# Optimization experiments

Measured on AMD Instinct MI355X. Metric: run time of the kernel, lower is better.

## Reference

```python
import jax, jax.numpy as jnp
import numpy as np

N, E = 50000, 200000
SIZES = [16, 32, 16]
EDIM = 8
EPS = 1e-5


def setup_inputs() -> dict:
    key = jax.random.key(0)
    ks = jax.random.split(key, 16)
    inp = {
        "x": jax.random.normal(ks[0], (N, SIZES[0]), jnp.float32),
        "edge_attr": jax.random.normal(ks[1], (E, EDIM), jnp.float32),
        "edge_index": jax.random.randint(ks[2], (2, E), 0, N, dtype=jnp.int32),
    }
    ki = 3
    for l in range(2):
        fin, fout = SIZES[l], SIZES[l + 1]
        m = fin * fout
        # xavier-ish init matching torch.nn.init.xavier_uniform_ scales
        inp[f"W1_{l}"] = jax.random.normal(ks[ki], (EDIM, m), jnp.float32) / np.float32(np.sqrt(EDIM)); ki += 1
        inp[f"b1_{l}"] = jnp.zeros((m,), jnp.float32)
        inp[f"W2_{l}"] = jax.random.normal(ks[ki], (m, m), jnp.float32) * np.float32(0.01 / np.sqrt(m)); ki += 1
        inp[f"b2_{l}"] = jnp.zeros((m,), jnp.float32)
        inp[f"root_{l}"] = jax.random.normal(ks[ki], (fin, fout), jnp.float32) / np.float32(np.sqrt(fin)); ki += 1
        inp[f"bias_{l}"] = jnp.zeros((fout,), jnp.float32)
        inp[f"gamma_{l}"] = jnp.ones((fout,), jnp.float32)
        inp[f"beta_{l}"] = jnp.zeros((fout,), jnp.float32)
    return inp


def _lrelu(v):
    return jnp.where(v >= 0, v, 0.01 * v)


def _nnconv(x, src, dst, edge_attr, W1, b1, W2, b2, root, bias, fin, fout):
    # edge MLP -> per-edge weight matrix [E, fin, fout]
    h = _lrelu(edge_attr @ W1 + b1) @ W2 + b2
    h = h.reshape(-1, fin, fout)
    # gather source node features, tiny per-edge matmul
    msg = jnp.einsum('ei,eio->eo', x[src], h)  # [E, fout]
    # scatter-mean aggregate at destination nodes
    agg = jax.ops.segment_sum(msg, dst, num_segments=N)
    deg = jax.ops.segment_sum(jnp.ones((msg.shape[0],), msg.dtype), dst, num_segments=N)
    agg = agg / jnp.maximum(deg, 1.0)[:, None]
    return agg + x @ root + bias


def _bn(v, gamma, beta):
    # BatchNorm1d (training mode: batch stats, biased variance)
    mu = v.mean(0)
    var = v.var(0)
    return (v - mu) * jax.lax.rsqrt(var + EPS) * gamma + beta


def reference(x, edge_attr,
              W1_0, b1_0, W2_0, b2_0, root_0, bias_0, gamma_0, beta_0,
              W1_1, b1_1, W2_1, b2_1, root_1, bias_1, gamma_1, beta_1,
              edge_index):
    src, dst = edge_index[0], edge_index[1]
    h = _nnconv(x, src, dst, edge_attr, W1_0, b1_0, W2_0, b2_0, root_0, bias_0, SIZES[0], SIZES[1])
    h = _lrelu(_bn(h, gamma_0, beta_0))
    h = _nnconv(h, src, dst, edge_attr, W1_1, b1_1, W2_1, b2_1, root_1, bias_1, SIZES[1], SIZES[2])
    return _bn(h, gamma_1, beta_1)
```

## Files before the change

kernel.cpp:

```cpp
#include <hip/hip_runtime.h>
#include <hip/hip_bf16.h>

typedef __attribute__((ext_vector_type(4))) float f32x4;
typedef __attribute__((ext_vector_type(8))) short s16x8;
typedef __attribute__((ext_vector_type(4))) int int4v;

#define DEVI __device__ __forceinline__

constexpr int NN = 50000;
constexpr int NE = 200000;
constexpr float BN_EPS = 1e-5f;

DEVI float lrelu_f(float v) { return v >= 0.f ? v : 0.01f * v; }

__global__ void k_transpose_w2(const float* __restrict__ W2, __hip_bfloat16* __restrict__ W2T) {
  __shared__ float tile[32][33];
  int bx = blockIdx.x % 16, by = blockIdx.x / 16;
  int t = threadIdx.x;
  int r = t / 32, c = t % 32;
  for (int rr = r; rr < 32; rr += 8)
    tile[rr][c] = W2[(size_t)(by * 32 + rr) * 512 + bx * 32 + c];
  __syncthreads();
  for (int rr = r; rr < 32; rr += 8)
    W2T[(size_t)(bx * 32 + rr) * 512 + by * 32 + c] = __float2bfloat16(tile[c][rr]);
}

__global__ void k_transpose_w1(const float* __restrict__ W1, __hip_bfloat16* __restrict__ W1T) {
  int tid = blockIdx.x * 256 + threadIdx.x;
  if (tid < 8 * 512) {
    int k = tid / 512, n = tid % 512;
    W1T[n * 8 + k] = __float2bfloat16(W1[tid]);
  }
}

__global__ void k_count(const int* __restrict__ dst, int* __restrict__ cnt) {
  int e = blockIdx.x * 256 + threadIdx.x;
  if (e < NE) atomicAdd(&cnt[dst[e]], 1);
}

constexpr int SCAN_ELEMS = 1024;
__global__ void k_scan1(const int* __restrict__ cnt, int* __restrict__ base, int* __restrict__ aux, int n) {
  __shared__ int sw[256];
  int b = blockIdx.x, t = threadIdx.x;
  int i0 = b * SCAN_ELEMS + t * 4;
  int v[4]; int s = 0;
  #pragma unroll
  for (int j = 0; j < 4; j++) { int idx = i0 + j; v[j] = (idx < n) ? cnt[idx] : 0; s += v[j]; }
  sw[t] = s; __syncthreads();
  for (int d = 1; d < 256; d <<= 1) {
    int val = (t >= d) ? sw[t - d] : 0;
    __syncthreads();
    sw[t] += val;
    __syncthreads();
  }
  int run = (t > 0) ? sw[t - 1] : 0;
  #pragma unroll
  for (int j = 0; j < 4; j++) { int idx = i0 + j; if (idx < n) base[idx] = run; run += v[j]; }
  if (t == 255) aux[b] = sw[255];
}

__global__ void k_scan2(int* aux, int nb) {
  if (threadIdx.x == 0 && blockIdx.x == 0) {
    int run = 0;
    for (int i = 0; i < nb; i++) { int v = aux[i]; aux[i] = run; run += v; }
  }
}

__global__ void k_scan3(int* __restrict__ base, int* __restrict__ cursor, const int* __restrict__ aux, int n) {
  int i = blockIdx.x * 256 + threadIdx.x;
  if (i < n) { int v = base[i] + aux[i / SCAN_ELEMS]; base[i] = v; cursor[i] = v; }
}

__global__ void k_place(const int* __restrict__ dst, int* __restrict__ cursor, int* __restrict__ perm) {
  int e = blockIdx.x * 256 + threadIdx.x;
  if (e < NE) { int p = atomicAdd(&cursor[dst[e]], 1); perm[p] = e; }
}

template <int FIN, int FOUT>
__global__ __launch_bounds__(512, 2)
void k_edge(const float* __restrict__ x, const float* __restrict__ ea,
            const int* __restrict__ srcI,
            const __hip_bfloat16* __restrict__ W1T, const float* __restrict__ b1,
            const __hip_bfloat16* __restrict__ W2T, const float* __restrict__ b2,
            __hip_bfloat16* __restrict__ msgb)
{
  static_assert(FOUT == 32 || FOUT == 16, "");
  constexpr int TM = 256;
  constexpr int CG = 32;
  constexpr int NCGI = 512 / CG;
  constexpr int NKC = 8;
  constexpr int NOT = FOUT / 16;
  constexpr int XPAD = 4;

  __shared__ __align__(16) char bbuf[2][CG * 512 * 2];
  __shared__ __align__(16) char gbuf[8][32 * 64 * 2];
  __shared__ __align__(16) __hip_bfloat16 eab[TM][8];
  __shared__ __align__(16) float xlf[TM][FIN + XPAD];

  const int tid = threadIdx.x;
  const int lane = tid & 63, w = tid >> 6;
  const int l15 = lane & 15, l4 = lane >> 4;
  const int e0 = blockIdx.x * TM;
  const int rem = min(TM, NE - e0);
  const int wrow0 = w * 32;

  if (tid < TM) {
    int er = e0 + min(tid, rem - 1);
    float4 v0 = *(const float4*)(ea + (size_t)er * 8);
    float4 v1 = *(const float4*)(ea + (size_t)er * 8 + 4);
    __hip_bfloat16* p = &eab[tid][0];
    p[0] = __float2bfloat16(v0.x); p[1] = __float2bfloat16(v0.y);
    p[2] = __float2bfloat16(v0.z); p[3] = __float2bfloat16(v0.w);
    p[4] = __float2bfloat16(v1.x); p[5] = __float2bfloat16(v1.y);
    p[6] = __float2bfloat16(v1.z); p[7] = __float2bfloat16(v1.w);
  }
  {
    constexpr int PRV = FIN / 4;
    for (int v = tid; v < TM * PRV; v += 512) {
      int row = v / PRV, q = v % PRV;
      int er = e0 + min(row, rem - 1);
      int s = srcI[er];
      *(float4*)(&xlf[row][q * 4]) = *(const float4*)(x + (size_t)s * FIN + q * 4);
    }
  }
  __syncthreads();

  s16x8 afe[2];
  #pragma unroll
  for (int rt = 0; rt < 2; rt++) {
    s16x8 tv = *(const s16x8*)(&eab[wrow0 + rt * 16 + l15][0]);
    afe[rt] = (lane < 16) ? tv : (s16x8)0;
  }
  char* gme = gbuf[w];
  s16x8 af[NKC][2][2];
  #pragma unroll
  for (int kc = 0; kc < NKC; kc++) {
    #pragma unroll
    for (int ct = 0; ct < 4; ct++) {
      int c = kc * 64 + ct * 16 + l15;
      s16x8 bw = *(const s16x8*)(W1T + c * 8);
      bw = (lane < 16) ? bw : (s16x8)0;
      float b1v = b1[c];
      #pragma unroll
      for (int rt = 0; rt < 2; rt++) {
        f32x4 d = __builtin_amdgcn_mfma_f32_16x16x32_bf16(afe[rt], bw, (f32x4)(0.f), 0, 0, 0);
        #pragma unroll
        for (int r = 0; r < 4; r++) {
          int rloc = rt * 16 + l4 * 4 + r;
          float gv = d[r] + b1v;
          gv = gv >= 0.f ? gv : 0.01f * gv;
          int byt = (rloc * 128 + (ct * 16 + l15) * 2) ^ ((rloc & 7) << 4);
          *(__hip_bfloat16*)(gme + byt) = __float2bfloat16(gv);
        }
      }
    }
    #pragma unroll
    for (int rt = 0; rt < 2; rt++)
      #pragma unroll
      for (int ks = 0; ks < 2; ks++) {
        int rloc = rt * 16 + l15;
        int byt = (rloc * 128 + (ks * 32 + l4 * 8) * 2) ^ ((rloc & 7) << 4);
        af[kc][rt][ks] = *(const s16x8*)(gme + byt);
      }
  }

  auto stage = [&](int cgi) {
    char* bb = bbuf[cgi & 1];
    int n = tid >> 4;
    int s0 = tid & 15;
    const char* gp = (const char*)(W2T + (size_t)(cgi * CG + n) * 512);
    #pragma unroll
    for (int j = 0; j < 4; j++) {
      int s = s0 + j * 16;
      *(int4v*)(&bb[n * 1024 + ((s ^ (n & 7)) << 4)]) = *(const int4v*)(gp + s * 16);
    }
  };

  f32x4 msg[2][NOT];
  #pragma unroll
  for (int rt = 0; rt < 2; rt++)
    #pragma unroll
    for (int ot = 0; ot < NOT; ot++) msg[rt][ot] = (f32x4)(0.f);

  stage(0);
  __syncthreads();

  for (int cgi = 0; cgi < NCGI; ++cgi) {
    if (cgi + 1 < NCGI) stage(cgi + 1);
    const char* bb = bbuf[cgi & 1];

    f32x4 acc[2][2];
    acc[0][0] = (f32x4)(0.f); acc[0][1] = (f32x4)(0.f);
    acc[1][0] = (f32x4)(0.f); acc[1][1] = (f32x4)(0.f);

    #pragma unroll
    for (int kc = 0; kc < NKC; kc++) {
      #pragma unroll
      for (int ct = 0; ct < 2; ct++) {
        int c = ct * 16 + l15;
        #pragma unroll
        for (int ks = 0; ks < 2; ks++) {
          int k = kc * 64 + ks * 32 + l4 * 8;
          s16x8 bw = *(const s16x8*)(&bb[(c * 1024 + k * 2) ^ ((c & 7) << 4)]);
          #pragma unroll
          for (int rt = 0; rt < 2; rt++)
            acc[rt][ct] = __builtin_amdgcn_mfma_f32_16x16x32_bf16(af[kc][rt][ks], bw, acc[rt][ct], 0, 0, 0);
        }
      }
    }

    #pragma unroll
    for (int ct = 0; ct < 2; ct++) {
      float b2v = b2[cgi * CG + ct * 16 + l15];
      const int iv = (FOUT == 32) ? cgi : (cgi * 2 + ct);
      const int ot = (FOUT == 32) ? ct : 0;
      #pragma unroll
      for (int rt = 0; rt < 2; rt++)
        #pragma unroll
        for (int r = 0; r < 4; r++) {
          int row = wrow0 + rt * 16 + l4 * 4 + r;
          msg[rt][ot][r] += xlf[row][iv] * (acc[rt][ct][r] + b2v);
        }
    }
    __syncthreads();
  }

  #pragma unroll
  for (int rt = 0; rt < 2; rt++)
    #pragma unroll
    for (int r = 0; r < 4; r++) {
      int row = wrow0 + rt * 16 + l4 * 4 + r;
      if (row < rem) {
        #pragma unroll
        for (int ot = 0; ot < NOT; ot++)
          msgb[(size_t)(e0 + row) * FOUT + ot * 16 + l15] = __float2bfloat16(msg[rt][ot][r]);
      }
    }
}

template <int FIN, int FOUT>
__global__ void k_node_agg(const __hip_bfloat16* __restrict__ msgb, const int* __restrict__ perm,
                           const int* __restrict__ base,
                           const float* __restrict__ x,
                           const float* __restrict__ root,
                           const float* __restrict__ bias,
                           float* __restrict__ h)
{
  __shared__ float rl[FIN * FOUT];
  constexpr int NPB = 256 / FOUT;
  int t = threadIdx.x;
  for (int i = t; i < FIN * FOUT; i += 256) rl[i] = root[i];
  __syncthreads();
  int n = blockIdx.x * NPB + t / FOUT;
  int o = t % FOUT;
  if (n >= NN) return;
  int s = base[n];
  int e = (n + 1 < NN) ? base[n + 1] : NE;
  float sum = 0.f;
  for (int j = s; j < e; j++)
    sum += __bfloat162float(msgb[(size_t)perm[j] * FOUT + o]);
  float acc = sum / fmaxf((float)(e - s), 1.f) + bias[o];
  #pragma unroll
  for (int i = 0; i < FIN; i++)
    acc += x[(size_t)n * FIN + i] * rl[i * FOUT + o];
  h[(size_t)n * FOUT + o] = acc;
}

template <int FOUT>
__global__ void k_stats(const float* __restrict__ h, float* __restrict__ ssum, float* __restrict__ ssq) {
  constexpr int RPB = 256 / FOUT;
  int t = threadIdx.x;
  int o = t % FOUT, rr = t / FOUT;
  float v = 0.f, v2 = 0.f;
  for (int r = blockIdx.x * RPB + rr; r < NN; r += gridDim.x * RPB) {
    float y = h[(size_t)r * FOUT + o];
    v += y; v2 += y * y;
  }
  #pragma unroll
  for (int d = FOUT; d < 64; d <<= 1) { v += __shfl_xor(v, d); v2 += __shfl_xor(v2, d); }
  __shared__ float sv[4][32], sq[4][32];
  int wv = t >> 6, ln = t & 63;
  if (ln < FOUT) { sv[wv][ln] = v; sq[wv][ln] = v2; }
  __syncthreads();
  if (t < FOUT) {
    float a = 0.f, b = 0.f;
    #pragma unroll
    for (int w2 = 0; w2 < 4; w2++) { a += sv[w2][t]; b += sq[w2][t]; }
    atomicAdd(&ssum[t], a);
    atomicAdd(&ssq[t], b);
  }
}

template <int FOUT, bool LRELU>
__global__ void k_bn(const float* __restrict__ h, const float* __restrict__ ssum,
                     const float* __restrict__ ssq, const float* __restrict__ gamma,
                     const float* __restrict__ beta, float* __restrict__ out)
{
  int idx = blockIdx.x * 256 + threadIdx.x;
  if (idx * 4 >= NN * FOUT) return;
  float4 v = *(const float4*)(h + (size_t)idx * 4);
  float r[4] = {v.x, v.y, v.z, v.w};
  #pragma unroll
  for (int j = 0; j < 4; j++) {
    int o = (idx * 4 + j) % FOUT;
    float mu = ssum[o] * (1.f / NN);
    float var = ssq[o] * (1.f / NN) - mu * mu;
    float sc = rsqrtf(var + BN_EPS) * gamma[o];
    float y = (r[j] - mu) * sc + beta[o];
    if (LRELU) y = lrelu_f(y);
    r[j] = y;
  }
  *(float4*)(out + (size_t)idx * 4) = make_float4(r[0], r[1], r[2], r[3]);
}

extern "C" void kernel_launch(void* const* d_in, const int* in_sizes, int n_in,
                              void* d_out, int out_size, void* d_ws, size_t ws_size,
                              hipStream_t stream)
{
  const float* x0    = (const float*)d_in[0];
  const float* ea    = (const float*)d_in[1];
  const int*   ei    = (const int*)d_in[2];
  const float* W1_0  = (const float*)d_in[3];
  const float* b1_0  = (const float*)d_in[4];
  const float* W2_0  = (const float*)d_in[5];
  const float* b2_0  = (const float*)d_in[6];
  const float* root0 = (const float*)d_in[7];
  const float* bias0 = (const float*)d_in[8];
  const float* gam0  = (const float*)d_in[9];
  const float* bet0  = (const float*)d_in[10];
  const float* W1_1  = (const float*)d_in[11];
  const float* b1_1  = (const float*)d_in[12];
  const float* W2_1  = (const float*)d_in[13];
  const float* b2_1  = (const float*)d_in[14];
  const float* root1 = (const float*)d_in[15];
  const float* bias1 = (const float*)d_in[16];
  const float* gam1  = (const float*)d_in[17];
  const float* bet1  = (const float*)d_in[18];
  const int* srcI = ei;
  const int* dstI = ei + NE;

  char* ws = (char*)d_ws;
  size_t off = 0;
  auto alloc = [&](size_t bytes) { char* p = ws + off; off += (bytes + 255) & ~(size_t)255; return p; };
  int*   cnt   = (int*)alloc(50048 * 4);
  float* ssum0 = (float*)alloc(32 * 4);
  float* ssq0  = (float*)alloc(32 * 4);
  float* ssum1 = (float*)alloc(16 * 4);
  float* ssq1  = (float*)alloc(16 * 4);
  size_t zero_bytes = off;
  int*   base   = (int*)alloc(50048 * 4);
  int*   cursor = (int*)alloc(50048 * 4);
  int*   aux    = (int*)alloc(64 * 4);
  int*   perm   = (int*)alloc((size_t)NE * 4);
  __hip_bfloat16* msgb = (__hip_bfloat16*)alloc((size_t)NE * 32 * 2);
  float* h0 = (float*)alloc((size_t)NN * 32 * 4);
  float* h1 = (float*)alloc((size_t)NN * 16 * 4);
  float* x1 = (float*)alloc((size_t)NN * 32 * 4);
  __hip_bfloat16* W2T0 = (__hip_bfloat16*)alloc(512 * 512 * 2);
  __hip_bfloat16* W2T1 = (__hip_bfloat16*)alloc(512 * 512 * 2);
  __hip_bfloat16* W1T0 = (__hip_bfloat16*)alloc(512 * 8 * 2);
  __hip_bfloat16* W1T1 = (__hip_bfloat16*)alloc(512 * 8 * 2);

  hipMemsetAsync(d_ws, 0, zero_bytes, stream);

  k_transpose_w2<<<256, 256, 0, stream>>>(W2_0, W2T0);
  k_transpose_w2<<<256, 256, 0, stream>>>(W2_1, W2T1);
  k_transpose_w1<<<16, 256, 0, stream>>>(W1_0, W1T0);
  k_transpose_w1<<<16, 256, 0, stream>>>(W1_1, W1T1);

  constexpr int NSB = (NN + SCAN_ELEMS - 1) / SCAN_ELEMS;
  k_count<<<(NE + 255) / 256, 256, 0, stream>>>(dstI, cnt);
  k_scan1<<<NSB, 256, 0, stream>>>(cnt, base, aux, NN);
  k_scan2<<<1, 64, 0, stream>>>(aux, NSB);
  k_scan3<<<(NN + 255) / 256, 256, 0, stream>>>(base, cursor, aux, NN);
  k_place<<<(NE + 255) / 256, 256, 0, stream>>>(dstI, cursor, perm);

  k_edge<16, 32><<<(NE + 255) / 256, 512, 0, stream>>>(x0, ea, srcI, W1T0, b1_0, W2T0, b2_0, msgb);
  k_node_agg<16, 32><<<(NN + 7) / 8, 256, 0, stream>>>(msgb, perm, base, x0, root0, bias0, h0);
  k_stats<32><<<128, 256, 0, stream>>>(h0, ssum0, ssq0);
  k_bn<32, true><<<((NN * 32 / 4) + 255) / 256, 256, 0, stream>>>(h0, ssum0, ssq0, gam0, bet0, x1);

  k_edge<32, 16><<<(NE + 255) / 256, 512, 0, stream>>>(x1, ea, srcI, W1T1, b1_1, W2T1, b2_1, msgb);
  k_node_agg<32, 16><<<(NN + 15) / 16, 256, 0, stream>>>(msgb, perm, base, x1, root1, bias1, h1);
  k_stats<16><<<128, 256, 0, stream>>>(h1, ssum1, ssq1);
  k_bn<16, false><<<((NN * 16 / 4) + 255) / 256, 256, 0, stream>>>(h1, ssum1, ssq1, gam1, bet1, (float*)d_out);
}
```

Baseline: 417.0 us.

## Double edge tile per block and split W2 K dimension into halves

The edge kernel now handles 512 edges per block (64 rows per wave) instead of 256, so each staged W2 chunk is reused across twice as many edges. To keep registers and LDS in budget, the 512-wide K of the second matmul is split into two 256-wide passes. The hidden-layer A fragments are regenerated per pass, and the W2 tiles are register-prefetched into a shared union buffer with padded strides. Gathered x is stored transposed in bf16, and the two weight-transpose launches per matrix are merged into one grid with blockIdx.y. The cost is more register pressure, bf16 rounding of x, and fewer blocks (391) for the GPU's CUs.

```diff
diff --git a/kernel.cpp b/kernel.cpp
--- a/kernel.cpp
+++ b/kernel.cpp
@@ -11,9 +11,13 @@
 constexpr int NE = 200000;
 constexpr float BN_EPS = 1e-5f;
 
+DEVI float bfbits2f(unsigned v) { union { unsigned u; float f; } t; t.u = v << 16; return t.f; }
 DEVI float lrelu_f(float v) { return v >= 0.f ? v : 0.01f * v; }
 
-__global__ void k_transpose_w2(const float* __restrict__ W2, __hip_bfloat16* __restrict__ W2T) {
+__global__ void k_transpose_w2(const float* __restrict__ A0, const float* __restrict__ A1,
+                               __hip_bfloat16* __restrict__ T0, __hip_bfloat16* __restrict__ T1) {
+  const float* W2 = blockIdx.y ? A1 : A0;
+  __hip_bfloat16* W2T = blockIdx.y ? T1 : T0;
   __shared__ float tile[32][33];
   int bx = blockIdx.x % 16, by = blockIdx.x / 16;
   int t = threadIdx.x;
@@ -25,7 +29,10 @@
     W2T[(size_t)(bx * 32 + rr) * 512 + by * 32 + c] = __float2bfloat16(tile[c][rr]);
 }
 
-__global__ void k_transpose_w1(const float* __restrict__ W1, __hip_bfloat16* __restrict__ W1T) {
+__global__ void k_transpose_w1(const float* __restrict__ A0, const float* __restrict__ A1,
+                               __hip_bfloat16* __restrict__ T0, __hip_bfloat16* __restrict__ T1) {
+  const float* W1 = blockIdx.y ? A1 : A0;
+  __hip_bfloat16* W1T = blockIdx.y ? T1 : T0;
   int tid = blockIdx.x * 256 + threadIdx.x;
   if (tid < 8 * 512) {
     int k = tid / 512, n = tid % 512;
@@ -85,26 +92,27 @@
             __hip_bfloat16* __restrict__ msgb)
 {
   static_assert(FOUT == 32 || FOUT == 16, "");
-  constexpr int TM = 256;
+  constexpr int TM = 512;
   constexpr int CG = 32;
-  constexpr int NCGI = 512 / CG;
-  constexpr int NKC = 8;
+  constexpr int NCGI = 16;
+  constexpr int KH = 256;
+  constexpr int NKC = 4;
   constexpr int NOT = FOUT / 16;
-  constexpr int XPAD = 4;
-
-  __shared__ __align__(16) char bbuf[2][CG * 512 * 2];
-  __shared__ __align__(16) char gbuf[8][32 * 64 * 2];
+  constexpr int BSTRIDE = KH * 2 + 16;
+  constexpr int XLDS = TM + 8;
+
+  __shared__ __align__(16) char ubuf[65536];
   __shared__ __align__(16) __hip_bfloat16 eab[TM][8];
-  __shared__ __align__(16) float xlf[TM][FIN + XPAD];
+  __shared__ __align__(16) __hip_bfloat16 xlt[FIN][XLDS];
 
   const int tid = threadIdx.x;
   const int lane = tid & 63, w = tid >> 6;
   const int l15 = lane & 15, l4 = lane >> 4;
   const int e0 = blockIdx.x * TM;
   const int rem = min(TM, NE - e0);
-  const int wrow0 = w * 32;
-
-  if (tid < TM) {
+  const int wrow0 = w * 64;
+
+  {
     int er = e0 + min(tid, rem - 1);
     float4 v0 = *(const float4*)(ea + (size_t)er * 8);
     float4 v1 = *(const float4*)(ea + (size_t)er * 8 + 4);
@@ -113,120 +121,140 @@
     p[2] = __float2bfloat16(v0.z); p[3] = __float2bfloat16(v0.w);
     p[4] = __float2bfloat16(v1.x); p[5] = __float2bfloat16(v1.y);
     p[6] = __float2bfloat16(v1.z); p[7] = __float2bfloat16(v1.w);
-  }
-  {
-    constexpr int PRV = FIN / 4;
-    for (int v = tid; v < TM * PRV; v += 512) {
-      int row = v / PRV, q = v % PRV;
-      int er = e0 + min(row, rem - 1);
-      int s = srcI[er];
-      *(float4*)(&xlf[row][q * 4]) = *(const float4*)(x + (size_t)s * FIN + q * 4);
+    int s = srcI[er];
+    #pragma unroll
+    for (int q = 0; q < FIN / 4; q++) {
+      float4 xv4 = *(const float4*)(x + (size_t)s * FIN + q * 4);
+      xlt[q * 4 + 0][tid] = __float2bfloat16(xv4.x);
+      xlt[q * 4 + 1][tid] = __float2bfloat16(xv4.y);
+      xlt[q * 4 + 2][tid] = __float2bfloat16(xv4.z);
+      xlt[q * 4 + 3][tid] = __float2bfloat16(xv4.w);
     }
   }
   __syncthreads();
 
-  s16x8 afe[2];
-  #pragma unroll
-  for (int rt = 0; rt < 2; rt++) {
-    s16x8 tv = *(const s16x8*)(&eab[wrow0 + rt * 16 + l15][0]);
-    afe[rt] = (lane < 16) ? tv : (s16x8)0;
-  }
-  char* gme = gbuf[w];
-  s16x8 af[NKC][2][2];
-  #pragma unroll
-  for (int kc = 0; kc < NKC; kc++) {
-    #pragma unroll
-    for (int ct = 0; ct < 4; ct++) {
-      int c = kc * 64 + ct * 16 + l15;
-      s16x8 bw = *(const s16x8*)(W1T + c * 8);
-      bw = (lane < 16) ? bw : (s16x8)0;
-      float b1v = b1[c];
-      #pragma unroll
-      for (int rt = 0; rt < 2; rt++) {
-        f32x4 d = __builtin_amdgcn_mfma_f32_16x16x32_bf16(afe[rt], bw, (f32x4)(0.f), 0, 0, 0);
-        #pragma unroll
-        for (int r = 0; r < 4; r++) {
-          int rloc = rt * 16 + l4 * 4 + r;
-          float gv = d[r] + b1v;
-          gv = gv >= 0.f ? gv : 0.01f * gv;
-          int byt = (rloc * 128 + (ct * 16 + l15) * 2) ^ ((rloc & 7) << 4);
-          *(__hip_bfloat16*)(gme + byt) = __float2bfloat16(gv);
+  f32x4 msg[4][NOT];
+  #pragma unroll
+  for (int rt = 0; rt < 4; rt++)
+    #pragma unroll
+    for (int ot = 0; ot < NOT; ot++) msg[rt][ot] = (f32x4)(0.f);
+
+  s16x8 af[NKC][4][2];
+  int4v sr0, sr1;
+
+  for (int sw = 0; sw < 2; ++sw) {
+    {
+      int n = tid >> 4, s0 = tid & 15;
+      const char* gp = (const char*)(W2T + (size_t)n * 512 + sw * KH);
+      sr0 = *(const int4v*)(gp + s0 * 16);
+      sr1 = *(const int4v*)(gp + (s0 + 16) * 16);
+    }
+    s16x8 afe[4];
+    #pragma unroll
+    for (int rt = 0; rt < 4; rt++) {
+      s16x8 tv = *(const s16x8*)(&eab[wrow0 + rt * 16 + l15][0]);
+      afe[rt] = (lane < 16) ? tv : (s16x8)0;
+    }
+    char* gme = ubuf + w * 8192;
+    #pragma unroll
+    for (int kc = 0; kc < NKC; kc++) {
+      #pragma unroll
+      for (int ct = 0; ct < 4; ct++) {
+        int c = sw * KH + kc * 64 + ct * 16 + l15;
+        s16x8 bw = *(const s16x8*)(W1T + c * 8);
+        bw = (lane < 16) ? bw : (s16x8)0;
+        float b1v = b1[c];
+        #pragma unroll
+        for (int rt = 0; rt < 4; rt++) {
+          f32x4 d = __builtin_amdgcn_mfma_f32_16x16x32_bf16(afe[rt], bw, (f32x4)(0.f), 0, 0, 0);
+          #pragma unroll
+          for (int r = 0; r < 4; r++) {
+            int rloc = rt * 16 + l4 * 4 + r;
+            float gv = d[r] + b1v;
+            gv = gv >= 0.f ? gv : 0.01f * gv;
+            int byt = (rloc * 128 + (ct * 16 + l15) * 2) ^ (((rloc + (rloc >> 2)) & 3) << 5);
+            *(__hip_bfloat16*)(gme + byt) = __float2bfloat16(gv);
+          }
         }
       }
-    }
-    #pragma unroll
-    for (int rt = 0; rt < 2; rt++)
-      #pragma unroll
-      for (int ks = 0; ks < 2; ks++) {
-        int rloc = rt * 16 + l15;
-        int byt = (rloc * 128 + (ks * 32 + l4 * 8) * 2) ^ ((rloc & 7) << 4);
-        af[kc][rt][ks] = *(const s16x8*)(gme + byt);
+      #pragma unroll
+      for (int rt = 0; rt < 4; rt++)
+        #pragma unroll
+        for (int ks = 0; ks < 2; ks++) {
+          int rloc = rt * 16 + l15;
+          int byt = (rloc * 128 + (ks * 32 + l4 * 8) * 2) ^ (((rloc + (rloc >> 2)) & 3) << 5);
+          af[kc][rt][ks] = *(const s16x8*)(gme + byt);
+        }
+    }
+    #pragma unroll
+    for (int kc = 0; kc < NKC; kc++)
+      #pragma unroll
+      for (int rt = 0; rt < 4; rt++)
+        #pragma unroll
+        for (int ks = 0; ks < 2; ks++)
+          asm volatile("" : "+v"(af[kc][rt][ks]));
+    __syncthreads();
+    {
+      int n = tid >> 4, s0 = tid & 15;
+      char* bb = ubuf;
+      *(int4v*)(bb + n * BSTRIDE + s0 * 16) = sr0;
+      *(int4v*)(bb + n * BSTRIDE + (s0 + 16) * 16) = sr1;
+    }
+    __syncthreads();
+
+    for (int cgi = 0; cgi < NCGI; ++cgi) {
+      if (cgi + 1 < NCGI) {
+        int n = tid >> 4, s0 = tid & 15;
+        const char* gp = (const char*)(W2T + (size_t)((cgi + 1) * CG + n) * 512 + sw * KH);
+        sr0 = *(const int4v*)(gp + s0 * 16);
+        sr1 = *(const int4v*)(gp + (s0 + 16) * 16);
       }
-  }
-
-  auto stage = [&](int cgi) {
-    char* bb = bbuf[cgi & 1];
-    int n = tid >> 4;
-    int s0 = tid & 15;
-    const char* gp = (const char*)(W2T + (size_t)(cgi * CG + n) * 512);
-    #pragma unroll
-    for (int j = 0; j < 4; j++) {
-      int s = s0 + j * 16;
-      *(int4v*)(&bb[n * 1024 + ((s ^ (n & 7)) << 4)]) = *(const int4v*)(gp + s * 16);
-    }
-  };
-
-  f32x4 msg[2][NOT];
-  #pragma unroll
-  for (int rt = 0; rt < 2; rt++)
-    #pragma unroll
-    for (int ot = 0; ot < NOT; ot++) msg[rt][ot] = (f32x4)(0.f);
-
-  stage(0);
-  __syncthreads();
-
-  for (int cgi = 0; cgi < NCGI; ++cgi) {
-    if (cgi + 1 < NCGI) stage(cgi + 1);
-    const char* bb = bbuf[cgi & 1];
-
-    f32x4 acc[2][2];
-    acc[0][0] = (f32x4)(0.f); acc[0][1] = (f32x4)(0.f);
-    acc[1][0] = (f32x4)(0.f); acc[1][1] = (f32x4)(0.f);
-
-    #pragma unroll
-    for (int kc = 0; kc < NKC; kc++) {
+      const char* bb = ubuf + (cgi & 1) * (CG * BSTRIDE);
+      f32x4 acc[4][2];
+      #pragma unroll
+      for (int rt = 0; rt < 4; rt++) { acc[rt][0] = (f32x4)(0.f); acc[rt][1] = (f32x4)(0.f); }
+
+      #pragma unroll
+      for (int kc = 0; kc < NKC; kc++)
+        #pragma unroll
+        for (int ct = 0; ct < 2; ct++) {
+          int c = ct * 16 + l15;
+          #pragma unroll
+          for (int ks = 0; ks < 2; ks++) {
+            const s16x8 bw = *(const s16x8*)(bb + c * BSTRIDE + kc * 128 + ks * 64 + l4 * 16);
+            #pragma unroll
+            for (int rt = 0; rt < 4; rt++)
+              acc[rt][ct] = __builtin_amdgcn_mfma_f32_16x16x32_bf16(af[kc][rt][ks], bw, acc[rt][ct], 0, 0, 0);
+          }
+        }
+
       #pragma unroll
       for (int ct = 0; ct < 2; ct++) {
-        int c = ct * 16 + l15;
-        #pragma unroll
-        for (int ks = 0; ks < 2; ks++) {
-          int k = kc * 64 + ks * 32 + l4 * 8;
-          s16x8 bw = *(const s16x8*)(&bb[(c * 1024 + k * 2) ^ ((c & 7) << 4)]);
-          #pragma unroll
-          for (int rt = 0; rt < 2; rt++)
-            acc[rt][ct] = __builtin_amdgcn_mfma_f32_16x16x32_bf16(af[kc][rt][ks], bw, acc[rt][ct], 0, 0, 0);
+        float b2v = (sw == 0) ? b2[cgi * CG + ct * 16 + l15] : 0.f;
+        const int iv = (FOUT == 32) ? cgi : (cgi * 2 + ct);
+        const int ot = (FOUT == 32) ? ct : 0;
+        #pragma unroll
+        for (int rt = 0; rt < 4; rt++) {
+          int rbase = wrow0 + rt * 16 + l4 * 4;
+          ushort4 xv = *(const ushort4*)(&xlt[iv][rbase]);
+          msg[rt][ot][0] += bfbits2f(xv.x) * (acc[rt][ct][0] + b2v);
+          msg[rt][ot][1] += bfbits2f(xv.y) * (acc[rt][ct][1] + b2v);
+          msg[rt][ot][2] += bfbits2f(xv.z) * (acc[rt][ct][2] + b2v);
+          msg[rt][ot][3] += bfbits2f(xv.w) * (acc[rt][ct][3] + b2v);
         }
       }
-    }
-
-    #pragma unroll
-    for (int ct = 0; ct < 2; ct++) {
-      float b2v = b2[cgi * CG + ct * 16 + l15];
-      const int iv = (FOUT == 32) ? cgi : (cgi * 2 + ct);
-      const int ot = (FOUT == 32) ? ct : 0;
-      #pragma unroll
-      for (int rt = 0; rt < 2; rt++)
-        #pragma unroll
-        for (int r = 0; r < 4; r++) {
-          int row = wrow0 + rt * 16 + l4 * 4 + r;
-          msg[rt][ot][r] += xlf[row][iv] * (acc[rt][ct][r] + b2v);
-        }
-    }
-    __syncthreads();
-  }
-
-  #pragma unroll
-  for (int rt = 0; rt < 2; rt++)
+      if (cgi + 1 < NCGI) {
+        int n = tid >> 4, s0 = tid & 15;
+        char* bw2 = ubuf + ((cgi + 1) & 1) * (CG * BSTRIDE);
+        *(int4v*)(bw2 + n * BSTRIDE + s0 * 16) = sr0;
+        *(int4v*)(bw2 + n * BSTRIDE + (s0 + 16) * 16) = sr1;
+      }
+      __syncthreads();
+    }
+  }
+
+  #pragma unroll
+  for (int rt = 0; rt < 4; rt++)
     #pragma unroll
     for (int r = 0; r < 4; r++) {
       int row = wrow0 + rt * 16 + l4 * 4 + r;
@@ -363,10 +391,8 @@
 
   hipMemsetAsync(d_ws, 0, zero_bytes, stream);
 
-  k_transpose_w2<<<256, 256, 0, stream>>>(W2_0, W2T0);
-  k_transpose_w2<<<256, 256, 0, stream>>>(W2_1, W2T1);
-  k_transpose_w1<<<16, 256, 0, stream>>>(W1_0, W1T0);
-  k_transpose_w1<<<16, 256, 0, stream>>>(W1_1, W1T1);
+  k_transpose_w2<<<dim3(256, 2), 256, 0, stream>>>(W2_0, W2_1, W2T0, W2T1);
+  k_transpose_w1<<<dim3(16, 2), 256, 0, stream>>>(W1_0, W1_1, W1T0, W1T1);
 
   constexpr int NSB = (NN + SCAN_ELEMS - 1) / SCAN_ELEMS;
   k_count<<<(NE + 255) / 256, 256, 0, stream>>>(dstI, cnt);
@@ -375,12 +401,13 @@
   k_scan3<<<(NN + 255) / 256, 256, 0, stream>>>(base, cursor, aux, NN);
   k_place<<<(NE + 255) / 256, 256, 0, stream>>>(dstI, cursor, perm);
 
-  k_edge<16, 32><<<(NE + 255) / 256, 512, 0, stream>>>(x0, ea, srcI, W1T0, b1_0, W2T0, b2_0, msgb);
+  constexpr int TM = 512;
+  k_edge<16, 32><<<(NE + TM - 1) / TM, 512, 0, stream>>>(x0, ea, srcI, W1T0, b1_0, W2T0, b2_0, msgb);
   k_node_agg<16, 32><<<(NN + 7) / 8, 256, 0, stream>>>(msgb, perm, base, x0, root0, bias0, h0);
   k_stats<32><<<128, 256, 0, stream>>>(h0, ssum0, ssq0);
   k_bn<32, true><<<((NN * 32 / 4) + 255) / 256, 256, 0, stream>>>(h0, ssum0, ssq0, gam0, bet0, x1);
 
-  k_edge<32, 16><<<(NE + 255) / 256, 512, 0, stream>>>(x1, ea, srcI, W1T1, b1_1, W2T1, b2_1, msgb);
+  k_edge<32, 16><<<(NE + TM - 1) / TM, 512, 0, stream>>>(x1, ea, srcI, W1T1, b1_1, W2T1, b2_1, msgb);
   k_node_agg<32, 16><<<(NN + 15) / 16, 256, 0, stream>>>(msgb, perm, base, x1, root1, bias1, h1);
   k_stats<16><<<128, 256, 0, stream>>>(h1, ssum1, ssq1);
   k_bn<16, false><<<((NN * 16 / 4) + 255) / 256, 256, 0, stream>>>(h1, ssum1, ssq1, gam1, bet1, (float*)d_out);
```

New measurement: 397.1 us. 4.8% less time.
